# Kernel optimization log

Hardware: AMD Instinct MI355X
Metric: run time of the kernel (lower is better)

Reference implementation:

```python
import jax, jax.numpy as jnp
import numpy as np


def _conv(x, w, b=None, pad=0):
    # x: [B,C,H,W], w: [O,I,kh,kw]
    y = jax.lax.conv_general_dilated(
        x, w, window_strides=(1, 1), padding=[(pad, pad), (pad, pad)],
        dimension_numbers=('NCHW', 'OIHW', 'NCHW'))
    if b is not None:
        y = y + b[None, :, None, None]
    return y


def _resb(x, w1, w2):
    h = _conv(x, w1, pad=1)
    h = jax.nn.leaky_relu(h, 0.1)
    h = _conv(h, w2, pad=1)
    return h + x


def setup_inputs() -> dict:
    key = jax.random.key(0)
    ks = jax.random.split(key, 16)
    B, C, H, W, K = 2, 64, 128, 256, 16
    s = 0.05
    return {
        'x_left': jax.random.normal(ks[0], (B, C, H, W), jnp.float32),
        'x_right': jax.random.normal(ks[1], (B, C, H, W), jnp.float32),
        'xxs': jax.random.randint(ks[2], (B, H * W, K), 0, H, jnp.int32),
        'yys': jax.random.randint(ks[3], (B, H * W, K), 0, W, jnp.int32),
        'is_training': 0,
        'rb_w1': jax.random.normal(ks[4], (C, C, 3, 3), jnp.float32) * s,
        'rb_w2': jax.random.normal(ks[5], (C, C, 3, 3), jnp.float32) * s,
        'b1_w': jax.random.normal(ks[6], (C, C, 1, 1), jnp.float32) * s,
        'b1_b': jax.random.normal(ks[7], (C,), jnp.float32) * s,
        'b2_w': jax.random.normal(ks[8], (C, C, 1, 1), jnp.float32) * s,
        'b2_b': jax.random.normal(ks[9], (C,), jnp.float32) * s,
        'b3_w': jax.random.normal(ks[10], (C, C, 1, 1), jnp.float32) * s,
        'b3_b': jax.random.normal(ks[11], (C,), jnp.float32) * s,
        'fus_w': jax.random.normal(ks[12], (C, 2 * C, 1, 1), jnp.float32) * s,
        'fus_b': jax.random.normal(ks[13], (C,), jnp.float32) * s,
    }


def reference(x_left, x_right, xxs, yys, is_training,
              rb_w1, rb_w2, b1_w, b1_b, b2_w, b2_b, b3_w, b3_b, fus_w, fus_b):
    B, C, H, W = x_left.shape
    HW = H * W
    K = xxs.shape[-1]

    buf_l = _resb(x_left, rb_w1, rb_w2)
    buf_r = _resb(x_right, rb_w1, rb_w2)

    Q = _conv(buf_l, b1_w, b1_b)   # [B,C,H,W]
    S = _conv(buf_r, b2_w, b2_b)
    R = _conv(buf_r, b3_w, b3_b)

    # per-pixel gather: S[b,:,Pos_x,Pos_y] -> flat index into H*W
    flat = (xxs.astype(jnp.int32) * W + yys.astype(jnp.int32)).reshape(B, HW * K)  # [B,HW*K]
    Sf = S.reshape(B, C, HW)
    Rf = R.reshape(B, C, HW)
    Key = jnp.take_along_axis(Sf, flat[:, None, :], axis=2).reshape(B, C, HW, K)
    Val = jnp.take_along_axis(Rf, flat[:, None, :], axis=2).reshape(B, C, HW, K)

    Qv = Q.transpose(0, 2, 3, 1).reshape(B, HW, C)           # [B,HW,C]
    score = jnp.einsum('bpc,bcpk->bpk', Qv, Key)             # [B,HW,K]
    M = jax.nn.softmax(score, axis=-1)                       # [B,HW,K]
    buf = jnp.einsum('bpk,bckp->bpc', M, Val.transpose(0, 1, 3, 2))  # [B,HW,C]
    buf = buf.reshape(B, H, W, C).transpose(0, 3, 1, 2)      # [B,C,H,W]

    out = _conv(jnp.concatenate([buf, x_left], axis=1), fus_w, fus_b)
    M_right_to_left = M[:, :, None, :]                       # [B,HW,1,K] as in torch
    if is_training == 1:
        return out
    return (out, M_right_to_left)
```

## Files before the change

### kernel.cpp

```cpp
#include <hip/hip_runtime.h>

#define HH 128
#define WW 256
#define CH 64
#define HWP (HH * WW)

typedef __attribute__((ext_vector_type(8))) __bf16 bf16x8;
typedef __attribute__((ext_vector_type(16))) float float16;

__device__ __forceinline__ unsigned short f2bf(float f) {
    unsigned u = __float_as_uint(f);
    u += 0x7fffu + ((u >> 16) & 1u);
    return (unsigned short)(u >> 16);
}
__device__ __forceinline__ float bf2f(unsigned short u) {
    return __uint_as_float((unsigned)u << 16);
}

__global__ __launch_bounds__(256) void prep_toT_k(
    const float* __restrict__ xl, const float* __restrict__ xr,
    const float* __restrict__ w1, const float* __restrict__ w2,
    const float* __restrict__ b1w, const float* __restrict__ b2w,
    const float* __restrict__ b3w, const float* __restrict__ fusw,
    unsigned short* __restrict__ XT, unsigned short* __restrict__ wB)
{
    const int tid = threadIdx.x;
    if (blockIdx.x < 2048) {
        __shared__ __align__(16) unsigned short sT[64 * 68];
        const int side = blockIdx.x >> 10;
        const int i0   = blockIdx.x & 1023;
        const int gp0  = i0 * 64;
        const int b    = gp0 >> 15;
        const int pofs = gp0 & (HWP - 1);
        const float* in = (side ? xr : xl) + (size_t)b * CH * HWP + pofs;

        for (int i = tid; i < 4096; i += 256) {
            int ci = i >> 6, px = i & 63;
            sT[px * 68 + ci] = f2bf(in[(size_t)ci * HWP + px]);
        }
        __syncthreads();
        const int px = tid >> 2, q = tid & 3;
        unsigned short* op = XT + ((size_t)(side * 2 + b) * HWP + pofs + px) * 64;
#pragma unroll
        for (int r = 0; r < 2; ++r)
            *(uint4*)&op[(q * 2 + r) * 8] = *(uint4*)&sT[px * 68 + (q * 2 + r) * 8];
        return;
    }

    int e = (blockIdx.x - 2048) * 256 + tid;
    float val;
    if (e < 73728) {
        const float* w = (e < 36864) ? w1 : w2;
        int t = (e < 36864) ? e : e - 36864;
        int j = t & 7, L = (t >> 3) & 63, nb = (t >> 9) & 1, kc = t >> 10;
        int k  = kc * 16 + (L >> 5) * 8 + j;
        int n  = nb * 32 + (L & 31);
        int kd = k >> 6, ci = k & 63;
        val = w[(n * 64 + ci) * 9 + kd];
    } else {
        int t = e - 73728;
        if (t < 4096) {
            int j = t & 7, L = (t >> 3) & 63, i3 = t >> 9;
            int nt = i3 & 1, kc = i3 >> 1;
            int n = nt * 32 + (L & 31), k = kc * 16 + (L >> 5) * 8 + j;
            val = b1w[n * 64 + k];
        } else if (t < 12288) {
            t -= 4096;
            int j = t & 7, L = (t >> 3) & 63, i3 = t >> 9;
            int nt = i3 & 3, kc = i3 >> 2;
            int n = nt * 32 + (L & 31), k = kc * 16 + (L >> 5) * 8 + j;
            val = (n < 64) ? b2w[n * 64 + k] : b3w[(n - 64) * 64 + k];
        } else {
            t -= 12288;
            int j = t & 7, L = (t >> 3) & 63, i3 = t >> 9;
            int nt = i3 & 1, kc = i3 >> 1;
            int n = nt * 32 + (L & 31), k = kc * 16 + (L >> 5) * 8 + j;
            val = fusw[n * 128 + k];
        }
    }
    wB[e] = f2bf(val);
}

__device__ __forceinline__ void stage_halo4(
    unsigned short* sA, const unsigned short* inT, int x0, int y0, int tid)
{
    for (int i = tid; i < 2112; i += 512) {
        int cell = i >> 3, j = i & 7;
        int row = cell / 66, col = cell - row * 66;
        int gy = y0 + row - 1, gx = x0 + col - 1;
        uint4 v = make_uint4(0, 0, 0, 0);
        if ((unsigned)gy < HH && (unsigned)gx < WW)
            v = *(const uint4*)&inT[(size_t)(gy * WW + gx) * 64 + j * 8];
        *(uint4*)&sA[(row * 66 + col) * 68 + j * 8] = v;
    }
}

__global__ __launch_bounds__(512) void conv1_k(
    const unsigned short* __restrict__ XT, const unsigned short* __restrict__ wB,
    unsigned short* __restrict__ H1T)
{
    __shared__ __align__(16) unsigned short sA[4 * 66 * 68];

    const int tid = threadIdx.x;
    const int x0  = blockIdx.x * 64;
    const int y0  = blockIdx.y * 2;
    const int sb  = blockIdx.z;
    const unsigned short* inT = XT + (size_t)sb * HWP * 64;

    stage_halo4(sA, inT, x0, y0, tid);
    __syncthreads();

    const int lane = tid & 63, wv = tid >> 6;
    const int rr = wv & 1, mw = (wv >> 1) & 1, nw = wv >> 2;
    const int m = lane & 31, kg = lane >> 5;
    const int pxl = mw * 32 + m;

    float16 acc;
#pragma unroll
    for (int i = 0; i < 16; ++i) acc[i] = 0.f;

#pragma unroll
    for (int kc = 0; kc < 36; ++kc) {
        const int kd = kc >> 2, hh = kc & 3;
        const int dy = kd / 3, dx = kd - dy * 3;
        bf16x8 af = *(const bf16x8*)&sA[((rr + dy) * 66 + pxl + dx) * 68 + hh * 16 + kg * 8];
        bf16x8 bf = *(const bf16x8*)&wB[((kc * 2 + nw) * 64 + lane) * 8];
        acc = __builtin_amdgcn_mfma_f32_32x32x16_bf16(af, bf, acc, 0, 0, 0);
    }

    __syncthreads();
    unsigned short* sCb = sA;
    const int n = nw * 32 + (lane & 31);
#pragma unroll
    for (int r = 0; r < 16; ++r) {
        int pr = rr * 64 + mw * 32 + (r & 3) + 8 * (r >> 2) + 4 * kg;
        float v = acc[r];
        v = v > 0.f ? v : 0.1f * v;
        sCb[pr * 68 + n] = f2bf(v);
    }
    __syncthreads();

    const int px2 = tid >> 2, q = tid & 3;
    const int orow = px2 >> 6, px = px2 & 63;
    unsigned short* op = H1T + ((size_t)sb * HWP + (y0 + orow) * WW + x0 + px) * 64 + q * 16;
    *(uint4*)&op[0] = *(uint4*)&sCb[px2 * 68 + q * 16];
    *(uint4*)&op[8] = *(uint4*)&sCb[px2 * 68 + q * 16 + 8];
}

__global__ __launch_bounds__(512) void conv2_k(
    const unsigned short* __restrict__ H1T, const unsigned short* __restrict__ XT,
    const unsigned short* __restrict__ wB2, const unsigned short* __restrict__ wQ,
    const unsigned short* __restrict__ wSR, const float* __restrict__ b1b,
    const float* __restrict__ b2b, const float* __restrict__ b3b,
    unsigned short* __restrict__ QT, unsigned short* __restrict__ ST,
    unsigned short* __restrict__ RT)
{
    __shared__ __align__(16) unsigned short sA[4 * 66 * 68];

    const int tid = threadIdx.x;
    const int x0  = blockIdx.x * 64;
    const int y0  = blockIdx.y * 2;
    const int sb  = blockIdx.z;
    const int side = sb >> 1, b = sb & 1;
    const unsigned short* inT = H1T + (size_t)sb * HWP * 64;

    stage_halo4(sA, inT, x0, y0, tid);
    __syncthreads();

    const int lane = tid & 63, wv = tid >> 6;
    const int rr = wv & 1, mw = (wv >> 1) & 1, nw = wv >> 2;
    const int m = lane & 31, kg = lane >> 5;
    const int pxl = mw * 32 + m;

    float16 acc;
#pragma unroll
    for (int i = 0; i < 16; ++i) acc[i] = 0.f;

#pragma unroll
    for (int kc = 0; kc < 36; ++kc) {
        const int kd = kc >> 2, hh = kc & 3;
        const int dy = kd / 3, dx = kd - dy * 3;
        bf16x8 af = *(const bf16x8*)&sA[((rr + dy) * 66 + pxl + dx) * 68 + hh * 16 + kg * 8];
        bf16x8 bf = *(const bf16x8*)&wB2[((kc * 2 + nw) * 64 + lane) * 8];
        acc = __builtin_amdgcn_mfma_f32_32x32x16_bf16(af, bf, acc, 0, 0, 0);
    }

    __syncthreads();
    unsigned short* sCb = sA;
    unsigned short* sC2 = sA + 8704;
    const int n = nw * 32 + (lane & 31);
    const unsigned short* xres = XT + (size_t)sb * HWP * 64;
#pragma unroll
    for (int r = 0; r < 16; ++r) {
        int pr = rr * 64 + mw * 32 + (r & 3) + 8 * (r >> 2) + 4 * kg;
        float xv = bf2f(xres[(size_t)((y0 + (pr >> 6)) * WW + x0 + (pr & 63)) * 64 + n]);
        sCb[pr * 68 + n] = f2bf(acc[r] + xv);
    }
    __syncthreads();

    const int px2 = tid >> 2, q = tid & 3;
    const int orow = px2 >> 6, px = px2 & 63;
    const size_t prow = (size_t)b * HWP + (y0 + orow) * WW + x0 + px;

    if (side == 0) {
        float16 a2;
#pragma unroll
        for (int i = 0; i < 16; ++i) a2[i] = 0.f;
#pragma unroll
        for (int kc = 0; kc < 4; ++kc) {
            bf16x8 af = *(const bf16x8*)&sCb[(rr * 64 + pxl) * 68 + kc * 16 + kg * 8];
            bf16x8 bf = *(const bf16x8*)&wQ[((kc * 2 + nw) * 64 + lane) * 8];
            a2 = __builtin_amdgcn_mfma_f32_32x32x16_bf16(af, bf, a2, 0, 0, 0);
        }
        float bv = b1b[n];
#pragma unroll
        for (int r = 0; r < 16; ++r) {
            int pr = rr * 64 + mw * 32 + (r & 3) + 8 * (r >> 2) + 4 * kg;
            sC2[pr * 68 + n] = f2bf(a2[r] + bv);
        }
        __syncthreads();
        unsigned short* op = QT + prow * 64 + q * 16;
        *(uint4*)&op[0] = *(uint4*)&sC2[px2 * 68 + q * 16];
        *(uint4*)&op[8] = *(uint4*)&sC2[px2 * 68 + q * 16 + 8];
    } else {
        float16 a2;
#pragma unroll
        for (int i = 0; i < 16; ++i) a2[i] = 0.f;
#pragma unroll
        for (int kc = 0; kc < 4; ++kc) {
            bf16x8 af = *(const bf16x8*)&sCb[(rr * 64 + pxl) * 68 + kc * 16 + kg * 8];
            bf16x8 bf = *(const bf16x8*)&wSR[((kc * 4 + nw) * 64 + lane) * 8];
            a2 = __builtin_amdgcn_mfma_f32_32x32x16_bf16(af, bf, a2, 0, 0, 0);
        }
        {
            float bv = b2b[n];
#pragma unroll
            for (int r = 0; r < 16; ++r) {
                int pr = rr * 64 + mw * 32 + (r & 3) + 8 * (r >> 2) + 4 * kg;
                sC2[pr * 68 + n] = f2bf(a2[r] + bv);
            }
        }
        __syncthreads();
        {
            unsigned short* op = ST + prow * 64 + q * 16;
            *(uint4*)&op[0] = *(uint4*)&sC2[px2 * 68 + q * 16];
            *(uint4*)&op[8] = *(uint4*)&sC2[px2 * 68 + q * 16 + 8];
        }
        __syncthreads();

#pragma unroll
        for (int i = 0; i < 16; ++i) a2[i] = 0.f;
#pragma unroll
        for (int kc = 0; kc < 4; ++kc) {
            bf16x8 af = *(const bf16x8*)&sCb[(rr * 64 + pxl) * 68 + kc * 16 + kg * 8];
            bf16x8 bf = *(const bf16x8*)&wSR[((kc * 4 + 2 + nw) * 64 + lane) * 8];
            a2 = __builtin_amdgcn_mfma_f32_32x32x16_bf16(af, bf, a2, 0, 0, 0);
        }
        {
            float bv = b3b[n];
#pragma unroll
            for (int r = 0; r < 16; ++r) {
                int pr = rr * 64 + mw * 32 + (r & 3) + 8 * (r >> 2) + 4 * kg;
                sC2[pr * 68 + n] = f2bf(a2[r] + bv);
            }
        }
        __syncthreads();
        {
            unsigned short* op = RT + prow * 64 + q * 16;
            *(uint4*)&op[0] = *(uint4*)&sC2[px2 * 68 + q * 16];
            *(uint4*)&op[8] = *(uint4*)&sC2[px2 * 68 + q * 16 + 8];
        }
    }
}

__global__ __launch_bounds__(512) void attn_fuse_k(
    const unsigned short* __restrict__ QT, const unsigned short* __restrict__ ST,
    const unsigned short* __restrict__ RT, const int* __restrict__ xxs,
    const int* __restrict__ yys, const unsigned short* __restrict__ XT,
    const unsigned short* __restrict__ wfrag, const float* __restrict__ bias,
    float* __restrict__ out, float* __restrict__ Mout)
{
    __shared__ __align__(16) unsigned char smem[64 * 68 * 4];
    unsigned short* sBuf = (unsigned short*)smem;
    unsigned short* sXT  = (unsigned short*)smem + 64 * 68;
    float*          sC   = (float*)smem;

    const int tid  = threadIdx.x;
    const int lane = tid & 63;
    const int wv   = tid >> 6;

    const int blk = blockIdx.x;
    const int b   = (blk & 4) ? 1 : 0;
    const int sub = (blk >> 3) * 4 + (blk & 3);
    const int pofs = sub * 64;
    const size_t gp0   = (size_t)b * HWP + pofs;
    const size_t bbase = (size_t)b * HWP;

    {
        const unsigned short* xlT = XT + gp0 * 64;
        int px = tid >> 3, j = tid & 7;
        *(uint4*)&sXT[px * 68 + j * 8] = *(const uint4*)&xlT[(size_t)px * 64 + j * 8];
    }

    const int k  = lane & 15, cq = lane >> 4;
    const unsigned short* rbase = RT + bbase * 64;
    const unsigned short* sbase = ST + bbase * 64;

    for (int it = 0; it < 8; ++it) {
        const int pl = wv * 8 + it;
        const size_t gp = gp0 + pl;

        const int flat = xxs[gp * 16 + k] * WW + yys[gp * 16 + k];

        uint4 sv0 = *(const uint4*)(sbase + (size_t)flat * 64 + cq * 16);
        uint4 sv1 = *(const uint4*)(sbase + (size_t)flat * 64 + cq * 16 + 8);
        uint4 qv0 = *(const uint4*)(QT + gp * 64 + cq * 16);
        uint4 qv1 = *(const uint4*)(QT + gp * 64 + cq * 16 + 8);

        unsigned short rv[16];
#pragma unroll
        for (int kk = 0; kk < 16; ++kk) {
            int fi = __builtin_amdgcn_readlane(flat, kk);
            rv[kk] = rbase[((unsigned)fi << 6) + lane];
        }

        float s0 = 0.f, s1 = 0.f;
        {
            const unsigned* sa  = (const unsigned*)&sv0;
            const unsigned* qa  = (const unsigned*)&qv0;
            const unsigned* sb2 = (const unsigned*)&sv1;
            const unsigned* qb2 = (const unsigned*)&qv1;
#pragma unroll
            for (int d = 0; d < 4; ++d) {
                s0 = fmaf(__uint_as_float(sa[d] << 16),
                          __uint_as_float(qa[d] << 16), s0);
                s0 = fmaf(__uint_as_float(sa[d] & 0xffff0000u),
                          __uint_as_float(qa[d] & 0xffff0000u), s0);
                s1 = fmaf(__uint_as_float(sb2[d] << 16),
                          __uint_as_float(qb2[d] << 16), s1);
                s1 = fmaf(__uint_as_float(sb2[d] & 0xffff0000u),
                          __uint_as_float(qb2[d] & 0xffff0000u), s1);
            }
        }
        float s = s0 + s1;
        s += __shfl_xor(s, 16, 64);
        s += __shfl_xor(s, 32, 64);

        const float e = __expf(s);

        float acc0 = 0.f, acc1 = 0.f;
#pragma unroll
        for (int kk = 0; kk < 8; ++kk) {
            float ea = __uint_as_float(
                __builtin_amdgcn_readlane(__float_as_uint(e), kk));
            float eb = __uint_as_float(
                __builtin_amdgcn_readlane(__float_as_uint(e), kk + 8));
            acc0 = fmaf(ea, bf2f(rv[kk]), acc0);
            acc1 = fmaf(eb, bf2f(rv[kk + 8]), acc1);
        }

        float sum = e;
#pragma unroll
        for (int mm = 1; mm <= 8; mm <<= 1) sum += __shfl_xor(sum, mm, 64);
        const float rinv = 1.f / sum;

        if (lane < 16) Mout[gp * 16 + lane] = e * rinv;
        sBuf[pl * 68 + lane] = f2bf((acc0 + acc1) * rinv);
    }
    __syncthreads();

    float16 facc;
#pragma unroll
    for (int i = 0; i < 16; ++i) facc[i] = 0.f;
    const int mw = wv & 1, nw = (wv >> 1) & 1;
    const int m = lane & 31, kg = lane >> 5;
    const int px_l = mw * 32 + m;

    if (tid < 256) {
#pragma unroll
        for (int kc = 0; kc < 8; ++kc) {
            const unsigned short* asrc = (kc < 4)
                ? &sBuf[px_l * 68 + kc * 16 + kg * 8]
                : &sXT[px_l * 68 + (kc - 4) * 16 + kg * 8];
            bf16x8 af = *(const bf16x8*)asrc;
            bf16x8 bf = *(const bf16x8*)&wfrag[((kc * 2 + nw) * 64 + lane) * 8];
            facc = __builtin_amdgcn_mfma_f32_32x32x16_bf16(af, bf, facc, 0, 0, 0);
        }
    }
    __syncthreads();

    if (tid < 256) {
        const int co_l = nw * 32 + (lane & 31);
#pragma unroll
        for (int r = 0; r < 16; ++r) {
            int pr = mw * 32 + (r & 3) + 8 * (r >> 2) + 4 * kg;
            sC[co_l * 68 + pr] = facc[r];
        }
    }
    __syncthreads();

    {
        const int co = tid >> 3, p0 = (tid & 7) * 8;
        const float bv = bias[co];
        float* op = out + ((size_t)b * CH + co) * HWP + pofs + p0;
#pragma unroll
        for (int q = 0; q < 2; ++q) {
            float4 v = *(float4*)&sC[co * 68 + p0 + q * 4];
            v.x += bv; v.y += bv; v.z += bv; v.w += bv;
            *(float4*)&op[q * 4] = v;
        }
    }
}

extern "C" void kernel_launch(void* const* d_in, const int* in_sizes, int n_in,
                              void* d_out, int out_size, void* d_ws, size_t ws_size,
                              hipStream_t stream)
{
    const float* x_left  = (const float*)d_in[0];
    const float* x_right = (const float*)d_in[1];
    const int*   xxs     = (const int*)d_in[2];
    const int*   yys     = (const int*)d_in[3];
    const float* rb_w1   = (const float*)d_in[5];
    const float* rb_w2   = (const float*)d_in[6];
    const float* b1_w    = (const float*)d_in[7];
    const float* b1_b    = (const float*)d_in[8];
    const float* b2_w    = (const float*)d_in[9];
    const float* b2_b    = (const float*)d_in[10];
    const float* b3_w    = (const float*)d_in[11];
    const float* b3_b    = (const float*)d_in[12];
    const float* fus_w   = (const float*)d_in[13];
    const float* fus_b   = (const float*)d_in[14];

    float* out  = (float*)d_out;
    float* Mout = out + (size_t)2 * CH * HWP;

    unsigned short* ws2 = (unsigned short*)d_ws;
    unsigned short* XT   = ws2;
    unsigned short* H1T  = ws2 + 8388608;
    unsigned short* QT   = ws2 + 16777216;
    unsigned short* ST   = ws2 + 20971520;
    unsigned short* RT   = ws2 + 25165824;
    unsigned short* wB   = ws2 + 29360128;

    prep_toT_k<<<2416, 256, 0, stream>>>(x_left, x_right, rb_w1, rb_w2,
                                         b1_w, b2_w, b3_w, fus_w, XT, wB);

    conv1_k<<<dim3(4, 64, 4), 512, 0, stream>>>(XT, wB, H1T);
    conv2_k<<<dim3(4, 64, 4), 512, 0, stream>>>(H1T, XT, wB + 36864, wB + 73728,
                                                wB + 77824, b1_b, b2_b, b3_b,
                                                QT, ST, RT);

    attn_fuse_k<<<1024, 512, 0, stream>>>(QT, ST, RT, xxs, yys, XT,
                                          wB + 86016, fus_b, out, Mout);
}
```

Measured before the change: 194.4 us.

## Halve attention block to 32 pixels, prefetch gather indices, use DPP reductions

The attention+fusion kernel now uses 256-thread blocks covering 32 pixels each, with twice as many blocks, and the final 1x1 conv MFMA runs on two waves instead of four. The next pixel's gather index is loaded one iteration ahead to hide index-load latency, and the 16-lane softmax sum uses DPP row operations instead of shuffles. The goal is better occupancy and latency hiding in this gather-bound kernel. The cost is fewer MFMA waves per block and a second read of the fusion weights by each extra block.

```diff
diff --git a/kernel.cpp b/kernel.cpp
--- a/kernel.cpp
+++ b/kernel.cpp
@@ -15,6 +15,11 @@
 }
 __device__ __forceinline__ float bf2f(unsigned short u) {
     return __uint_as_float((unsigned)u << 16);
+}
+template <int CTRL>
+__device__ __forceinline__ float dpp_add(float x) {
+    int t = __builtin_amdgcn_update_dpp(0, __float_as_int(x), CTRL, 0xF, 0xF, true);
+    return x + __int_as_float(t);
 }
 
 __global__ __launch_bounds__(256) void prep_toT_k(
@@ -273,16 +278,16 @@
     }
 }
 
-__global__ __launch_bounds__(512) void attn_fuse_k(
+__global__ __launch_bounds__(256) void attn_fuse_k(
     const unsigned short* __restrict__ QT, const unsigned short* __restrict__ ST,
     const unsigned short* __restrict__ RT, const int* __restrict__ xxs,
     const int* __restrict__ yys, const unsigned short* __restrict__ XT,
     const unsigned short* __restrict__ wfrag, const float* __restrict__ bias,
     float* __restrict__ out, float* __restrict__ Mout)
 {
-    __shared__ __align__(16) unsigned char smem[64 * 68 * 4];
+    __shared__ __align__(16) unsigned char smem[9216];
     unsigned short* sBuf = (unsigned short*)smem;
-    unsigned short* sXT  = (unsigned short*)smem + 64 * 68;
+    unsigned short* sXT  = (unsigned short*)smem + 32 * 68;
     float*          sC   = (float*)smem;
 
     const int tid  = threadIdx.x;
@@ -292,7 +297,7 @@
     const int blk = blockIdx.x;
     const int b   = (blk & 4) ? 1 : 0;
     const int sub = (blk >> 3) * 4 + (blk & 3);
-    const int pofs = sub * 64;
+    const int pofs = sub * 32;
     const size_t gp0   = (size_t)b * HWP + pofs;
     const size_t bbase = (size_t)b * HWP;
 
@@ -306,11 +311,13 @@
     const unsigned short* rbase = RT + bbase * 64;
     const unsigned short* sbase = ST + bbase * 64;
 
+    size_t gp = gp0 + wv * 8;
+    int flat = xxs[gp * 16 + k] * WW + yys[gp * 16 + k];
+
     for (int it = 0; it < 8; ++it) {
-        const int pl = wv * 8 + it;
-        const size_t gp = gp0 + pl;
-
-        const int flat = xxs[gp * 16 + k] * WW + yys[gp * 16 + k];
+        int nflat = 0;
+        if (it < 7)
+            nflat = xxs[(gp + 1) * 16 + k] * WW + yys[(gp + 1) * 16 + k];
 
         uint4 sv0 = *(const uint4*)(sbase + (size_t)flat * 64 + cq * 16);
         uint4 sv1 = *(const uint4*)(sbase + (size_t)flat * 64 + cq * 16 + 8);
@@ -360,23 +367,28 @@
         }
 
         float sum = e;
-#pragma unroll
-        for (int mm = 1; mm <= 8; mm <<= 1) sum += __shfl_xor(sum, mm, 64);
+        sum = dpp_add<0xB1>(sum);
+        sum = dpp_add<0x4E>(sum);
+        sum = dpp_add<0x141>(sum);
+        sum = dpp_add<0x140>(sum);
         const float rinv = 1.f / sum;
 
         if (lane < 16) Mout[gp * 16 + lane] = e * rinv;
-        sBuf[pl * 68 + lane] = f2bf((acc0 + acc1) * rinv);
+        sBuf[(wv * 8 + it) * 68 + lane] = f2bf((acc0 + acc1) * rinv);
+
+        flat = nflat;
+        ++gp;
     }
     __syncthreads();
 
     float16 facc;
 #pragma unroll
     for (int i = 0; i < 16; ++i) facc[i] = 0.f;
-    const int mw = wv & 1, nw = (wv >> 1) & 1;
-    const int m = lane & 31, kg = lane >> 5;
-    const int px_l = mw * 32 + m;
-
-    if (tid < 256) {
+    const int nw = wv;
+    const int kg = lane >> 5;
+    const int px_l = lane & 31;
+
+    if (tid < 128) {
 #pragma unroll
         for (int kc = 0; kc < 8; ++kc) {
             const unsigned short* asrc = (kc < 4)
@@ -389,23 +401,23 @@
     }
     __syncthreads();
 
-    if (tid < 256) {
+    if (tid < 128) {
         const int co_l = nw * 32 + (lane & 31);
 #pragma unroll
         for (int r = 0; r < 16; ++r) {
-            int pr = mw * 32 + (r & 3) + 8 * (r >> 2) + 4 * kg;
-            sC[co_l * 68 + pr] = facc[r];
+            int pr = (r & 3) + 8 * (r >> 2) + 4 * kg;
+            sC[co_l * 36 + pr] = facc[r];
         }
     }
     __syncthreads();
 
     {
-        const int co = tid >> 3, p0 = (tid & 7) * 8;
+        const int co = tid >> 2, p0 = (tid & 3) * 8;
         const float bv = bias[co];
         float* op = out + ((size_t)b * CH + co) * HWP + pofs + p0;
 #pragma unroll
         for (int q = 0; q < 2; ++q) {
-            float4 v = *(float4*)&sC[co * 68 + p0 + q * 4];
+            float4 v = *(float4*)&sC[co * 36 + p0 + q * 4];
             v.x += bv; v.y += bv; v.z += bv; v.w += bv;
             *(float4*)&op[q * 4] = v;
         }
@@ -450,6 +462,6 @@
                                                 wB + 77824, b1_b, b2_b, b3_b,
                                                 QT, ST, RT);
 
-    attn_fuse_k<<<1024, 512, 0, stream>>>(QT, ST, RT, xxs, yys, XT,
+    attn_fuse_k<<<2048, 256, 0, stream>>>(QT, ST, RT, xxs, yys, XT,
                                           wB + 86016, fus_b, out, Mout);
 }
```

After: 189.9 us. 1.02x faster.
